# Kernel tuning notes

Measured on AMD Instinct MI355X. Metric: run time of the kernel, lower is better.

Reference implementation:

```python
import jax, jax.numpy as jnp
import numpy as np

B, N, K = 4, 4096, 16
C_IN = 128
EPS = 1e-5


def setup_inputs() -> dict:
    key = jax.random.key(0)
    ks = jax.random.split(key, 8)
    c0 = 2 * C_IN + 3  # concat channels: pos_diff(3) + feat2(128) + feat1(128)
    return {
        "pos1": jax.random.normal(ks[0], (B, 3, N), jnp.float32),
        "pos2": jax.random.normal(ks[1], (B, 3, N), jnp.float32),
        "feature1": jax.random.normal(ks[2], (B, C_IN, N), jnp.float32),
        "feature2": jax.random.normal(ks[3], (B, C_IN, N), jnp.float32),
        "W0": jax.random.normal(ks[4], (128, c0), jnp.float32) * 0.05,
        "W1": jax.random.normal(ks[5], (128, 128), jnp.float32) * 0.05,
        "W2": jax.random.normal(ks[6], (128, 128), jnp.float32) * 0.05,
        "g0": jnp.ones((128,), jnp.float32),
        "g1": jnp.ones((128,), jnp.float32),
        "g2": jnp.ones((128,), jnp.float32),
        "b0": jnp.zeros((128,), jnp.float32),
        "b1": jnp.zeros((128,), jnp.float32),
        "b2": jnp.zeros((128,), jnp.float32),
    }


def _knn_idx(pos1, pos2, k):
    # pos1, pos2: (B, 3, N).  For each point in pos1, k nearest points in pos2.
    p1 = pos1.transpose(0, 2, 1)  # (B, N, 3)
    p2 = pos2.transpose(0, 2, 1)  # (B, M, 3)
    d = (jnp.sum(p1 * p1, -1, keepdims=True)
         + jnp.sum(p2 * p2, -1)[:, None, :]
         - 2.0 * jnp.einsum("bnc,bmc->bnm", p1, p2))  # (B, N, M) squared dists
    _, idx = jax.lax.top_k(-d, k)  # (B, N, K)
    return idx


def _group(x, idx):
    # x: (B, C, M), idx: (B, N, K) -> (B, C, N, K)
    xt = x.transpose(0, 2, 1)  # (B, M, C)
    g = jax.vmap(lambda a, i: a[i])(xt, idx)  # (B, N, K, C)
    return g.transpose(0, 3, 1, 2)


def _conv_bn_relu(x, W, g, b):
    # 1x1 conv (no bias) + BatchNorm2d (training: batch stats, biased var) + ReLU
    y = jnp.einsum("oc,bcnk->bonk", W, x)
    mu = jnp.mean(y, axis=(0, 2, 3), keepdims=True)
    var = jnp.var(y, axis=(0, 2, 3), keepdims=True)
    yn = (y - mu) * jax.lax.rsqrt(var + EPS)
    return jax.nn.relu(yn * g[None, :, None, None] + b[None, :, None, None])


def reference(pos1, pos2, feature1, feature2, W0, W1, W2, g0, g1, g2, b0, b1, b2):
    idx = _knn_idx(pos1, pos2, K)                      # (B, N, K)
    pos2_g = _group(pos2, idx)                         # (B, 3, N, K)
    pos_diff = pos2_g - pos1[:, :, :, None]
    feat2_g = _group(feature2, idx)                    # (B, C, N, K)
    feat1_rep = jnp.broadcast_to(feature1[:, :, :, None], (B, C_IN, N, K))
    x = jnp.concatenate([pos_diff, feat2_g, feat1_rep], axis=1)  # (B, 2C+3, N, K)
    x = _conv_bn_relu(x, W0, g0, b0)
    x = _conv_bn_relu(x, W1, g1, b1)
    x = _conv_bn_relu(x, W2, g2, b2)
    feat1_new = jnp.max(x, axis=-1)                    # (B, mlp[-1], N)
    return (pos1, feat1_new)
```

## Files before the change

### kernel.cpp

```cpp
#include <hip/hip_runtime.h>

#define B_ 4
#define N_ 4096
#define K_ 16
#define C_ 128
#define NQ (B_*N_)
#define COLS_TOT (NQ*K_)
#define CNT_F 262144.0f
#define EPS_ 1e-5f

typedef __attribute__((ext_vector_type(8))) short short8;
typedef __attribute__((ext_vector_type(4))) float f4;
typedef __attribute__((ext_vector_type(4))) int i4;

__device__ __forceinline__ unsigned short f2bf(float f){
  unsigned u = __builtin_bit_cast(unsigned, f);
  u = u + 0x7fffu + ((u >> 16) & 1u);
  return (unsigned short)(u >> 16);
}
__device__ __forceinline__ float bf2f(unsigned short h){
  return __builtin_bit_cast(float, ((unsigned)h) << 16);
}
__device__ __forceinline__ int swzc(int c){ return c ^ ((c >> 3) & 7); }

__global__ __launch_bounds__(256) void wconv(
    const float* __restrict__ W0, const float* __restrict__ W1, const float* __restrict__ W2,
    unsigned short* __restrict__ W0b, unsigned short* __restrict__ W0c,
    unsigned short* __restrict__ W1b, unsigned short* __restrict__ W2b)
{
  int i = blockIdx.x * 256 + threadIdx.x;
  int sel = i >> 14, r = i & 16383;
  int o = r >> 7, c = r & 127;
  float v; unsigned short* dst;
  if (sel == 0)      { v = W0[o*259 + 3   + c]; dst = W0b; }
  else if (sel == 1) { v = W0[o*259 + 131 + c]; dst = W0c; }
  else if (sel == 2) { v = W1[o*128 + c];       dst = W1b; }
  else               { v = W2[o*128 + c];       dst = W2b; }
  dst[r] = f2bf(v);
}

__global__ __launch_bounds__(256) void knn_chunk(
    const float* __restrict__ pos1, const float* __restrict__ pos2,
    float* __restrict__ kdout, int* __restrict__ kiout)
{
  __shared__ __align__(16) float pts[256*4];
  int bx = blockIdx.x;
  int b = bx >> 8, rest = bx & 255, ngrp = rest >> 4, chunk = rest & 15;
  int t = threadIdx.x;
  int m0 = chunk * 256;
  const float* p2 = pos2 + (size_t)b*3*N_;
  {
    int m = m0 + t;
    float x = p2[m], y = p2[N_ + m], z = p2[2*N_ + m];
    float sq = __fadd_rn(__fadd_rn(__fmul_rn(x,x), __fmul_rn(y,y)), __fmul_rn(z,z));
    f4 v; v.x = x; v.y = y; v.z = z; v.w = sq;
    *(f4*)(pts + t*4) = v;
  }
  __syncthreads();

  int n = ngrp*256 + t;
  const float* p1 = pos1 + (size_t)b*3*N_;
  float qx = p1[n], qy = p1[N_ + n], qz = p1[2*N_ + n];
  float qs = __fadd_rn(__fadd_rn(__fmul_rn(qx,qx), __fmul_rn(qy,qy)), __fmul_rn(qz,qz));

  float kd[16]; int ki[16];
  #pragma unroll
  for (int j = 0; j < 16; ++j){ kd[j] = 3.4e38f; ki[j] = 0; }
  float worst = 3.4e38f;
  float pd = 0.f; int pi = 0; bool pv = false;

  auto flush = [&](){
    float d0 = pv ? pd : 3.4e38f; int i0 = pi;
    #pragma unroll
    for (int j = 15; j >= 1; --j){
      bool cj = kd[j] > d0, cm = kd[j-1] > d0;
      kd[j] = cj ? (cm ? kd[j-1] : d0) : kd[j];
      ki[j] = cj ? (cm ? ki[j-1] : i0) : ki[j];
    }
    { bool c0 = kd[0] > d0; kd[0] = c0 ? d0 : kd[0]; ki[0] = c0 ? i0 : ki[0]; }
    worst = kd[15]; pv = false;
  };

  for (int bt = 0; bt < 32; ++bt){
    #pragma unroll
    for (int e = 0; e < 8; ++e){
      int it = bt*8 + e;
      f4 c = *(const f4*)(pts + it*4);
      float dot = __builtin_fmaf(qz, c.z,
                    __builtin_fmaf(qy, c.y, __fmul_rn(qx, c.x)));
      float d = __fsub_rn(__fadd_rn(qs, c.w), __fmul_rn(2.0f, dot));
      bool pass = d < worst;
      if (__any(pass && pv)) flush();
      if (pass){ pd = d; pi = m0 + it; pv = true; }
    }
    if (__any(pv)) flush();
  }
  if (__any(pv)) flush();

  int q = b*N_ + n;
  #pragma unroll
  for (int j = 0; j < 16; ++j){
    kdout[(size_t)q*256 + chunk*16 + j] = kd[j];
    kiout[(size_t)q*256 + chunk*16 + j] = ki[j];
  }
}

__global__ __launch_bounds__(256) void knn_merge(
    const float* __restrict__ kdin, const int* __restrict__ kiin, int* __restrict__ idxout)
{
  int q = blockIdx.x*256 + threadIdx.x;
  float kd[16]; int ki[16];
  #pragma unroll
  for (int j = 0; j < 16; ++j){ kd[j] = 3.4e38f; ki[j] = 0; }
  const float* dsrc = kdin + (size_t)q*256;
  const int*   isrc = kiin + (size_t)q*256;
  for (int l = 0; l < 16; ++l){
    bool dead = false;
    #pragma unroll 1
    for (int s4 = 0; s4 < 4; ++s4){
      if (__all(dead)) break;
      f4 dv = *(const f4*)(dsrc + l*16 + s4*4);
      i4 iv = *(const i4*)(isrc + l*16 + s4*4);
      #pragma unroll
      for (int e = 0; e < 4; ++e){
        float d0 = dv[e]; int i0 = iv[e];
        bool ins = !dead && (kd[15] > d0);
        dead = dead || !ins;
        if (ins){
          #pragma unroll
          for (int j = 15; j >= 1; --j){
            bool cj = kd[j] > d0, cm = kd[j-1] > d0;
            kd[j] = cj ? (cm ? kd[j-1] : d0) : kd[j];
            ki[j] = cj ? (cm ? ki[j-1] : i0) : ki[j];
          }
          bool c0 = kd[0] > d0; kd[0] = c0 ? d0 : kd[0]; ki[0] = c0 ? i0 : ki[0];
        }
      }
    }
  }
  #pragma unroll
  for (int j = 0; j < 16; ++j) idxout[(size_t)q*16 + j] = ki[j];
}

__global__ __launch_bounds__(256) void p1_gemm(
    const float* __restrict__ feat2, const float* __restrict__ feat1,
    const unsigned short* __restrict__ W0b, const unsigned short* __restrict__ W0c,
    float* __restrict__ F2t, float* __restrict__ PREt)
{
  __shared__ __align__(16) unsigned short X[16*128*8];
  int bid = blockIdx.x;
  int sel = bid >> 7;
  const float* src = sel ? feat1 : feat2;
  const unsigned short* W = sel ? W0c : W0b;
  float* dst = sel ? PREt : F2t;
  int c0 = (bid & 127) * 128;
  int b = c0 >> 12, mm0 = c0 & 4095;
  int t = threadIdx.x;
  {
    int ch = t >> 1, half = t & 1;
    const float* s = src + ((size_t)b*C_ + ch)*N_ + mm0 + half*64;
    int kb = ch >> 3, e = ch & 7;
    for (int mi = 0; mi < 64; ++mi){
      int col = half*64 + mi;
      X[kb*1024 + swzc(col)*8 + e] = f2bf(s[mi]);
    }
  }
  int lane = t & 63, w = t >> 6;
  int or0 = (w >> 1)*64, c0w = (w & 1)*64;
  int lr = lane & 15, lg = lane >> 4;
  short8 af[4][4];
  #pragma unroll
  for (int ks = 0; ks < 4; ++ks)
    #pragma unroll
    for (int i = 0; i < 4; ++i)
      af[ks][i] = *(const short8*)(W + (or0 + 16*i + lr)*128 + ks*32 + 8*lg);
  __syncthreads();

  f4 acc[4][4] = {};
  #pragma unroll
  for (int ks = 0; ks < 4; ++ks){
    short8 bfr[4];
    #pragma unroll
    for (int j = 0; j < 4; ++j)
      bfr[j] = *(const short8*)(X + (ks*4 + lg)*1024 + swzc(c0w + 16*j + lr)*8);
    #pragma unroll
    for (int i = 0; i < 4; ++i)
      #pragma unroll
      for (int j = 0; j < 4; ++j)
        acc[i][j] = __builtin_amdgcn_mfma_f32_16x16x32_bf16(af[ks][i], bfr[j], acc[i][j], 0, 0, 0);
  }
  #pragma unroll
  for (int i = 0; i < 4; ++i)
    #pragma unroll
    for (int j = 0; j < 4; ++j){
      int col = c0 + c0w + 16*j + lr;
      *(f4*)(dst + (size_t)col*C_ + or0 + 16*i + 4*lg) = acc[i][j];
    }
}

__global__ __launch_bounds__(256) void k3_stats(
    const float* __restrict__ pos1, const float* __restrict__ pos2,
    const float* __restrict__ W0, const int* __restrict__ idx,
    const float* __restrict__ F2t, const float* __restrict__ PREt,
    float* __restrict__ partials)
{
  __shared__ float w0a[384];
  __shared__ float ldsS[256];
  int t = threadIdx.x;
  for (int i = t; i < 384; i += 256) w0a[i] = W0[(i/3)*259 + (i%3)];
  __syncthreads();
  int cloc = t & 15, chg = t >> 4, ch0 = chg*8;
  float wx[8], wy[8], wz[8];
  #pragma unroll
  for (int e = 0; e < 8; ++e){
    wx[e] = w0a[(ch0+e)*3]; wy[e] = w0a[(ch0+e)*3+1]; wz[e] = w0a[(ch0+e)*3+2];
  }
  float s1[8] = {}, s2[8] = {};
  int base = blockIdx.x * 256;
  for (int it = 0; it < 16; ++it){
    int col = base + it*16 + cloc;
    int nabs = col >> 4;
    int b = nabs >> 12, n = nabs & 4095;
    int m = idx[col];
    float dx = pos2[(size_t)(b*3+0)*N_ + m] - pos1[(size_t)(b*3+0)*N_ + n];
    float dy = pos2[(size_t)(b*3+1)*N_ + m] - pos1[(size_t)(b*3+1)*N_ + n];
    float dz = pos2[(size_t)(b*3+2)*N_ + m] - pos1[(size_t)(b*3+2)*N_ + n];
    const float* f2 = F2t  + ((size_t)b*N_ + m)*C_ + ch0;
    const float* pr = PREt + ((size_t)b*N_ + n)*C_ + ch0;
    #pragma unroll
    for (int e = 0; e < 8; ++e){
      float y = f2[e] + pr[e];
      y = fmaf(wx[e], dx, y); y = fmaf(wy[e], dy, y); y = fmaf(wz[e], dz, y);
      s1[e] += y; s2[e] = fmaf(y, y, s2[e]);
    }
  }
  #pragma unroll
  for (int e = 0; e < 8; ++e){
    float a = s1[e], q = s2[e];
    #pragma unroll
    for (int sft = 1; sft < 16; sft <<= 1){ a += __shfl_xor(a, sft); q += __shfl_xor(q, sft); }
    if (cloc == 0){ ldsS[ch0 + e] = a; ldsS[128 + ch0 + e] = q; }
  }
  __syncthreads();
  partials[(size_t)blockIdx.x*256 + t] = ldsS[t];
}

__global__ __launch_bounds__(256) void reduce1(const float* __restrict__ partials,
                                               float* __restrict__ partial2)
{
  int t = threadIdx.x, r0 = blockIdx.x*32;
  float a = 0.f;
  #pragma unroll 4
  for (int i = 0; i < 32; ++i) a += partials[(size_t)(r0+i)*256 + t];
  partial2[(size_t)blockIdx.x*256 + t] = a;
}

__global__ __launch_bounds__(256) void finalize(const float* __restrict__ partial2, int rows,
    const float* __restrict__ g, const float* __restrict__ bb,
    float* __restrict__ cA, float* __restrict__ cB)
{
  __shared__ float sh[256];
  int t = threadIdx.x;
  float a = 0.f;
  for (int i = 0; i < rows; ++i) a += partial2[(size_t)i*256 + t];
  sh[t] = a;
  __syncthreads();
  if (t < 128){
    float mu = sh[t] / CNT_F;
    float var = sh[128 + t] / CNT_F - mu*mu;
    float A = g[t] * rsqrtf(var + EPS_);
    cA[t] = A; cB[t] = bb[t] - mu*A;
  }
}

__global__ __launch_bounds__(256,2) void layer1_fused(
    const float* __restrict__ pos1, const float* __restrict__ pos2,
    const float* __restrict__ W0, const int* __restrict__ idx,
    const float* __restrict__ F2t, const float* __restrict__ PREt,
    unsigned short* __restrict__ ybuf,
    const unsigned short* __restrict__ Wbf,
    const float* __restrict__ cA, const float* __restrict__ cB,
    float* __restrict__ partials)
{
  __shared__ __align__(16) char lds[40960];
  unsigned short* X = (unsigned short*)lds;
  float* ldsA = (float*)(lds + 32768);
  float* ldsB = ldsA + 128;
  float* w0a  = ldsB + 128;
  float* ldsS = w0a + 384;
  int t = threadIdx.x;
  int c0 = blockIdx.x * 128;
  if (t < 128){ ldsA[t] = cA[t]; ldsB[t] = cB[t]; }
  for (int i = t; i < 384; i += 256) w0a[i] = W0[(i/3)*259 + (i%3)];
  ldsS[t] = 0.f; ldsS[256 + t] = 0.f;
  __syncthreads();

  int lane = t & 63, w = t >> 6;
  int or0 = (w >> 1)*64, c0w = (w & 1)*64;
  int lr = lane & 15, lg = lane >> 4;

  {
    int colL = t >> 1, half = t & 1;
    int col = c0 + colL;
    int nabs = col >> 4;
    int b = nabs >> 12, n = nabs & 4095;
    int m = idx[col];
    float dx = pos2[(size_t)(b*3+0)*N_ + m] - pos1[(size_t)(b*3+0)*N_ + n];
    float dy = pos2[(size_t)(b*3+1)*N_ + m] - pos1[(size_t)(b*3+1)*N_ + n];
    float dz = pos2[(size_t)(b*3+2)*N_ + m] - pos1[(size_t)(b*3+2)*N_ + n];
    const float* f2 = F2t  + ((size_t)b*N_ + m)*C_ + half*64;
    const float* pr = PREt + ((size_t)b*N_ + n)*C_ + half*64;
    int sc = swzc(colL);
    #pragma unroll
    for (int cc = 0; cc < 8; ++cc){
      int ch0 = half*64 + cc*8;
      f4 a0 = *(const f4*)(f2 + cc*8), a1 = *(const f4*)(f2 + cc*8 + 4);
      f4 b0 = *(const f4*)(pr + cc*8), b1 = *(const f4*)(pr + cc*8 + 4);
      short8 xv;
      #pragma unroll
      for (int e = 0; e < 8; ++e){
        int ch = ch0 + e;
        float fv = (e < 4 ? a0[e] : a1[e-4]);
        float pv = (e < 4 ? b0[e] : b1[e-4]);
        float y = fv + pv;
        y = fmaf(w0a[ch*3], dx, y); y = fmaf(w0a[ch*3+1], dy, y); y = fmaf(w0a[ch*3+2], dz, y);
        float v = fmaf(y, ldsA[ch], ldsB[ch]);
        v = v > 0.f ? v : 0.f;
        xv[e] = (short)f2bf(v);
      }
      *(short8*)(X + (ch0 >> 3)*1024 + sc*8) = xv;
    }
  }

  short8 af[4][4];
  #pragma unroll
  for (int ks = 0; ks < 4; ++ks)
    #pragma unroll
    for (int i = 0; i < 4; ++i)
      af[ks][i] = *(const short8*)(Wbf + (or0 + 16*i + lr)*128 + ks*32 + 8*lg);
  __syncthreads();

  f4 acc[4][4] = {};
  #pragma unroll
  for (int ks = 0; ks < 4; ++ks){
    short8 bfr[4];
    #pragma unroll
    for (int j = 0; j < 4; ++j)
      bfr[j] = *(const short8*)(X + (ks*4 + lg)*1024 + swzc(c0w + 16*j + lr)*8);
    #pragma unroll
    for (int i = 0; i < 4; ++i)
      #pragma unroll
      for (int j = 0; j < 4; ++j)
        acc[i][j] = __builtin_amdgcn_mfma_f32_16x16x32_bf16(af[ks][i], bfr[j], acc[i][j], 0, 0, 0);
  }

  #pragma unroll
  for (int i = 0; i < 4; ++i)
    #pragma unroll
    for (int e = 0; e < 4; ++e){
      float a0 = acc[i][0][e], a1 = acc[i][1][e], a2 = acc[i][2][e], a3 = acc[i][3][e];
      float s1 = (a0 + a1) + (a2 + a3);
      float s2 = (a0*a0 + a1*a1) + (a2*a2 + a3*a3);
      #pragma unroll
      for (int sft = 1; sft < 16; sft <<= 1){ s1 += __shfl_xor(s1, sft); s2 += __shfl_xor(s2, sft); }
      if (lr == 0){
        int o = or0 + 16*i + 4*lg + e;
        ldsS[(w & 1)*256 + o] = s1;
        ldsS[(w & 1)*256 + 128 + o] = s2;
      }
    }

  __syncthreads();
  unsigned short* OT = (unsigned short*)lds;
  #pragma unroll
  for (int i = 0; i < 4; ++i)
    #pragma unroll
    for (int j = 0; j < 4; ++j){
      int col = c0w + 16*j + lr;
      int o0 = or0 + 16*i + 4*lg;
      unsigned long long pv =
          (unsigned long long)f2bf(acc[i][j][0])
        | ((unsigned long long)f2bf(acc[i][j][1]) << 16)
        | ((unsigned long long)f2bf(acc[i][j][2]) << 32)
        | ((unsigned long long)f2bf(acc[i][j][3]) << 48);
      *(unsigned long long*)(OT + col*136 + o0) = pv;
    }
  __syncthreads();
  {
    int colL = t >> 1, half = t & 1;
    unsigned short* dst = ybuf + (size_t)(c0 + colL)*128 + half*64;
    #pragma unroll
    for (int cc = 0; cc < 8; ++cc){
      short8 v = *(const short8*)(OT + colL*136 + half*64 + cc*8);
      *(short8*)(dst + cc*8) = v;
    }
  }
  __syncthreads();
  partials[(size_t)blockIdx.x*256 + t] = ldsS[t] + ldsS[256 + t];
}

__global__ __launch_bounds__(256,2) void layer_gemm_last(
    unsigned short* ybuf,
    const unsigned short* __restrict__ Wbf,
    const float* __restrict__ cA, const float* __restrict__ cB,
    float* __restrict__ y2max,
    float* __restrict__ partials)
{
  __shared__ __align__(16) char lds[38912];
  unsigned short* X = (unsigned short*)lds;
  float* ldsA = (float*)(lds + 34816);
  float* ldsB = ldsA + 128;
  float* ldsS = ldsB + 128;
  int t = threadIdx.x;
  int c0 = blockIdx.x * 128;
  if (t < 128){ ldsA[t] = cA[t]; ldsB[t] = cB[t]; }
  ldsS[t] = 0.f; ldsS[256 + t] = 0.f;

  int lane = t & 63, w = t >> 6;
  int or0 = (w >> 1)*64, c0w = (w & 1)*64;
  int lr = lane & 15, lg = lane >> 4;
  short8 af[4][4];
  #pragma unroll
  for (int ks = 0; ks < 4; ++ks)
    #pragma unroll
    for (int i = 0; i < 4; ++i)
      af[ks][i] = *(const short8*)(Wbf + (or0 + 16*i + lr)*128 + ks*32 + 8*lg);
  __syncthreads();

  {
    int colL = t >> 1, half = t & 1;
    const unsigned short* src = ybuf + (size_t)(c0 + colL)*128 + half*64;
    int sc = swzc(colL);
    #pragma unroll
    for (int cc = 0; cc < 8; ++cc){
      int ch0 = half*64 + cc*8;
      short8 yv = *(const short8*)(src + cc*8);
      short8 xv;
      #pragma unroll
      for (int e = 0; e < 8; ++e){
        float f = bf2f((unsigned short)yv[e]);
        float v = fmaf(f, ldsA[ch0 + e], ldsB[ch0 + e]);
        v = v > 0.f ? v : 0.f;
        xv[e] = (short)f2bf(v);
      }
      *(short8*)(X + (ch0 >> 3)*1024 + sc*8) = xv;
    }
  }
  __syncthreads();

  f4 acc[4][4] = {};
  #pragma unroll
  for (int ks = 0; ks < 4; ++ks){
    short8 bfr[4];
    #pragma unroll
    for (int j = 0; j < 4; ++j)
      bfr[j] = *(const short8*)(X + (ks*4 + lg)*1024 + swzc(c0w + 16*j + lr)*8);
    #pragma unroll
    for (int i = 0; i < 4; ++i)
      #pragma unroll
      for (int j = 0; j < 4; ++j)
        acc[i][j] = __builtin_amdgcn_mfma_f32_16x16x32_bf16(af[ks][i], bfr[j], acc[i][j], 0, 0, 0);
  }

  #pragma unroll
  for (int i = 0; i < 4; ++i)
    #pragma unroll
    for (int e = 0; e < 4; ++e){
      float a0 = acc[i][0][e], a1 = acc[i][1][e], a2 = acc[i][2][e], a3 = acc[i][3][e];
      float s1 = (a0 + a1) + (a2 + a3);
      float s2 = (a0*a0 + a1*a1) + (a2*a2 + a3*a3);
      #pragma unroll
      for (int sft = 1; sft < 16; sft <<= 1){ s1 += __shfl_xor(s1, sft); s2 += __shfl_xor(s2, sft); }
      if (lr == 0){
        int o = or0 + 16*i + 4*lg + e;
        ldsS[(w & 1)*256 + o] = s1;
        ldsS[(w & 1)*256 + 128 + o] = s2;
      }
    }

  float keep[4][4] = {};
  #pragma unroll
  for (int j = 0; j < 4; ++j)
    #pragma unroll
    for (int i = 0; i < 4; ++i)
      #pragma unroll
      for (int e = 0; e < 4; ++e){
        float v = acc[i][j][e];
        #pragma unroll
        for (int sft = 1; sft < 16; sft <<= 1) v = fmaxf(v, __shfl_xor(v, sft));
        if (lr == j) keep[i][e] = v;
      }
  if (lr < 4){
    int colg = c0 + c0w + 16*lr;
    int nabs = colg >> 4;
    float* dst = y2max + (size_t)nabs*C_;
    #pragma unroll
    for (int i = 0; i < 4; ++i){
      f4 v; v.x = keep[i][0]; v.y = keep[i][1]; v.z = keep[i][2]; v.w = keep[i][3];
      *(f4*)(dst + or0 + 16*i + 4*lg) = v;
    }
  }
  __syncthreads();
  partials[(size_t)blockIdx.x*256 + t] = ldsS[t] + ldsS[256 + t];
}

__global__ __launch_bounds__(256) void k7_out(
    const float* __restrict__ y2max, const float* __restrict__ cA,
    const float* __restrict__ cB, float* __restrict__ outF)
{
  __shared__ __align__(16) float T[128*65];
  int t = threadIdx.x, bid = blockIdx.x;
  int b = bid >> 6, n0 = (bid & 63)*64;
  {
    int nl = t >> 2, o0 = (t & 3)*32;
    const float* src = y2max + ((size_t)b*N_ + n0 + nl)*C_ + o0;
    #pragma unroll
    for (int jj = 0; jj < 8; ++jj){
      f4 v = *(const f4*)(src + jj*4);
      T[(o0 + jj*4 + 0)*65 + nl] = v.x;
      T[(o0 + jj*4 + 1)*65 + nl] = v.y;
      T[(o0 + jj*4 + 2)*65 + nl] = v.z;
      T[(o0 + jj*4 + 3)*65 + nl] = v.w;
    }
  }
  __syncthreads();
  {
    int o = t >> 1, half = t & 1;
    float A = cA[o], Bb = cB[o];
    float* dst = outF + ((size_t)b*C_ + o)*N_ + n0 + half*32;
    #pragma unroll
    for (int jj = 0; jj < 8; ++jj){
      f4 v;
      float x0 = fmaf(T[o*65 + half*32 + jj*4+0], A, Bb);
      float x1 = fmaf(T[o*65 + half*32 + jj*4+1], A, Bb);
      float x2 = fmaf(T[o*65 + half*32 + jj*4+2], A, Bb);
      float x3 = fmaf(T[o*65 + half*32 + jj*4+3], A, Bb);
      v.x = x0 > 0.f ? x0 : 0.f; v.y = x1 > 0.f ? x1 : 0.f;
      v.z = x2 > 0.f ? x2 : 0.f; v.w = x3 > 0.f ? x3 : 0.f;
      *(f4*)(dst + jj*4) = v;
    }
  }
}

extern "C" void kernel_launch(void* const* d_in, const int* in_sizes, int n_in,
                              void* d_out, int out_size, void* d_ws, size_t ws_size,
                              hipStream_t stream)
{
  (void)in_sizes; (void)n_in; (void)out_size; (void)ws_size;
  const float* pos1  = (const float*)d_in[0];
  const float* pos2  = (const float*)d_in[1];
  const float* feat1 = (const float*)d_in[2];
  const float* feat2 = (const float*)d_in[3];
  const float* W0 = (const float*)d_in[4];
  const float* W1 = (const float*)d_in[5];
  const float* W2 = (const float*)d_in[6];
  const float* g0 = (const float*)d_in[7];
  const float* g1 = (const float*)d_in[8];
  const float* g2 = (const float*)d_in[9];
  const float* b0 = (const float*)d_in[10];
  const float* b1 = (const float*)d_in[11];
  const float* b2 = (const float*)d_in[12];

  char* ws = (char*)d_ws;
  size_t off = 0;
  auto alloc = [&](size_t bytes){ size_t r = off; off += (bytes + 255) & ~(size_t)255; return r; };
  int*   idx     = (int*)  (ws + alloc((size_t)COLS_TOT*4));
  float* F2t     = (float*)(ws + alloc((size_t)NQ*C_*4));
  float* PREt    = (float*)(ws + alloc((size_t)NQ*C_*4));
  unsigned short* ybuf = (unsigned short*)(ws + alloc((size_t)COLS_TOT*C_*2));
  float* y2max   = (float*)(ws + alloc((size_t)NQ*C_*4));
  float* partials= (float*)(ws + alloc((size_t)2048*256*4));
  float* partial2= (float*)(ws + alloc((size_t)64*256*4));
  float* coef    = (float*)(ws + alloc((size_t)6*128*4));
  unsigned short* W0bb = (unsigned short*)(ws + alloc(16384*2));
  unsigned short* W0cb = (unsigned short*)(ws + alloc(16384*2));
  unsigned short* W1b  = (unsigned short*)(ws + alloc(16384*2));
  unsigned short* W2b  = (unsigned short*)(ws + alloc(16384*2));

  float* knn_d = (float*)ybuf;
  int*   knn_i = (int*)((char*)ybuf + (size_t)NQ*256*4);

  float* cA0 = coef,       *cB0 = coef + 128;
  float* cA1 = coef + 256, *cB1 = coef + 384;
  float* cA2 = coef + 512, *cB2 = coef + 640;

  wconv<<<256, 256, 0, stream>>>(W0, W1, W2, W0bb, W0cb, W1b, W2b);
  knn_chunk<<<1024, 256, 0, stream>>>(pos1, pos2, knn_d, knn_i);
  knn_merge<<<64, 256, 0, stream>>>(knn_d, knn_i, idx);
  p1_gemm<<<256, 256, 0, stream>>>(feat2, feat1, W0bb, W0cb, F2t, PREt);
  k3_stats<<<1024, 256, 0, stream>>>(pos1, pos2, W0, idx, F2t, PREt, partials);
  reduce1<<<32, 256, 0, stream>>>(partials, partial2);
  finalize<<<1, 256, 0, stream>>>(partial2, 32, g0, b0, cA0, cB0);
  layer1_fused<<<2048, 256, 0, stream>>>(pos1, pos2, W0, idx, F2t, PREt,
                                          ybuf, W1b, cA0, cB0, partials);
  reduce1<<<64, 256, 0, stream>>>(partials, partial2);
  finalize<<<1, 256, 0, stream>>>(partial2, 64, g1, b1, cA1, cB1);
  layer_gemm_last<<<2048, 256, 0, stream>>>(ybuf, W2b, cA1, cB1, y2max, partials);
  reduce1<<<64, 256, 0, stream>>>(partials, partial2);
  finalize<<<1, 256, 0, stream>>>(partial2, 64, g2, b2, cA2, cB2);
  k7_out<<<256, 256, 0, stream>>>(y2max, cA2, cB2, (float*)d_out + (size_t)B_*3*N_);
  hipMemcpyAsync(d_out, d_in[0], (size_t)B_*3*N_*4, hipMemcpyDeviceToDevice, stream);
}
```

Measured before the change: 417.9 us.

## Transpose kNN partial-result layout for coalesced access and coalesce p1_gemm loads

```diff
diff --git a/kernel.cpp b/kernel.cpp
--- a/kernel.cpp
+++ b/kernel.cpp
@@ -100,8 +100,8 @@
   int q = b*N_ + n;
   #pragma unroll
   for (int j = 0; j < 16; ++j){
-    kdout[(size_t)q*256 + chunk*16 + j] = kd[j];
-    kiout[(size_t)q*256 + chunk*16 + j] = ki[j];
+    kdout[(size_t)(chunk*16 + j)*NQ + q] = kd[j];
+    kiout[(size_t)(chunk*16 + j)*NQ + q] = ki[j];
   }
 }
 
@@ -112,26 +112,27 @@
   float kd[16]; int ki[16];
   #pragma unroll
   for (int j = 0; j < 16; ++j){ kd[j] = 3.4e38f; ki[j] = 0; }
-  const float* dsrc = kdin + (size_t)q*256;
-  const int*   isrc = kiin + (size_t)q*256;
+  #pragma unroll 1
   for (int l = 0; l < 16; ++l){
+    float dv[16]; int iv[16];
+    #pragma unroll
+    for (int j = 0; j < 16; ++j){
+      dv[j] = kdin[(size_t)(l*16 + j)*NQ + q];
+      iv[j] = kiin[(size_t)(l*16 + j)*NQ + q];
+    }
     bool dead = false;
-    #pragma unroll 1
-    for (int s4 = 0; s4 < 4; ++s4){
-      if (__all(dead)) break;
-      f4 dv = *(const f4*)(dsrc + l*16 + s4*4);
-      i4 iv = *(const i4*)(isrc + l*16 + s4*4);
-      #pragma unroll
-      for (int e = 0; e < 4; ++e){
-        float d0 = dv[e]; int i0 = iv[e];
-        bool ins = !dead && (kd[15] > d0);
-        dead = dead || !ins;
+    #pragma unroll
+    for (int j = 0; j < 16; ++j){
+      bool ins = !dead && (kd[15] > dv[j]);
+      dead = !ins;
+      if (__any(ins)){
         if (ins){
+          float d0 = dv[j]; int i0 = iv[j];
           #pragma unroll
-          for (int j = 15; j >= 1; --j){
-            bool cj = kd[j] > d0, cm = kd[j-1] > d0;
-            kd[j] = cj ? (cm ? kd[j-1] : d0) : kd[j];
-            ki[j] = cj ? (cm ? ki[j-1] : i0) : ki[j];
+          for (int jj = 15; jj >= 1; --jj){
+            bool cj = kd[jj] > d0, cm = kd[jj-1] > d0;
+            kd[jj] = cj ? (cm ? kd[jj-1] : d0) : kd[jj];
+            ki[jj] = cj ? (cm ? ki[jj-1] : i0) : ki[jj];
           }
           bool c0 = kd[0] > d0; kd[0] = c0 ? d0 : kd[0]; ki[0] = c0 ? i0 : ki[0];
         }
@@ -139,7 +140,10 @@
     }
   }
   #pragma unroll
-  for (int j = 0; j < 16; ++j) idxout[(size_t)q*16 + j] = ki[j];
+  for (int j = 0; j < 4; ++j){
+    i4 v; v.x = ki[j*4]; v.y = ki[j*4+1]; v.z = ki[j*4+2]; v.w = ki[j*4+3];
+    *(i4*)(idxout + (size_t)q*16 + j*4) = v;
+  }
 }
 
 __global__ __launch_bounds__(256) void p1_gemm(
@@ -157,12 +161,12 @@
   int b = c0 >> 12, mm0 = c0 & 4095;
   int t = threadIdx.x;
   {
-    int ch = t >> 1, half = t & 1;
-    const float* s = src + ((size_t)b*C_ + ch)*N_ + mm0 + half*64;
-    int kb = ch >> 3, e = ch & 7;
-    for (int mi = 0; mi < 64; ++mi){
-      int col = half*64 + mi;
-      X[kb*1024 + swzc(col)*8 + e] = f2bf(s[mi]);
+    int colt = t & 127, chh = t >> 7;
+    #pragma unroll 4
+    for (int it = 0; it < 64; ++it){
+      int ch = it*2 + chh;
+      float v = src[((size_t)b*C_ + ch)*N_ + mm0 + colt];
+      X[(ch >> 3)*1024 + swzc(colt)*8 + (ch & 7)] = f2bf(v);
     }
   }
   int lane = t & 63, w = t >> 6;
```

New measurement: 424.3 us. No clear change (+1.5%).
